# Performance work log

Hardware: AMD Instinct MI355X
Metric: run time of the kernel (lower is better)

The kernel has to match this reference:

```python
import jax, jax.numpy as jnp
import numpy as np

VOCAB = 256
EMB = 512
B, T = 64, 1024


def setup_inputs() -> dict:
    key = jax.random.key(0)
    ks = jax.random.split(key, 7)
    s_emb = 1.0  # nn.Embedding default init N(0,1)
    lim_cell = 1.0 / np.sqrt(2 * EMB)  # Linear default U(-1/sqrt(fan_in), ...)
    lim_head = 1.0 / np.sqrt(EMB)
    return {
        "x": jax.random.randint(ks[0], (B, T), 0, VOCAB),
        "emb": jax.random.normal(ks[1], (VOCAB, EMB), dtype=jnp.float32) * s_emb,
        "w_cell": jax.random.uniform(ks[2], (EMB, 2 * EMB), jnp.float32, -lim_cell, lim_cell),
        "b_cell": jax.random.uniform(ks[3], (EMB,), jnp.float32, -lim_cell, lim_cell),
        "w_head": jax.random.uniform(ks[4], (VOCAB, EMB), jnp.float32, -lim_head, lim_head),
        "b_head": jax.random.uniform(ks[5], (VOCAB,), jnp.float32, -lim_head, lim_head),
        "h0": jnp.zeros((1, EMB), jnp.float32),
    }


def reference(x, emb, w_cell, b_cell, w_head, b_head, h0):
    # x: [B,T] int -> embedded [B,T,E]
    xe = emb[x]
    e = emb.shape[1]
    # cell: tanh(cat(x_t, h) @ W^T + b); split W into x-part and h-part
    w_x, w_h = w_cell[:, :e], w_cell[:, e:]
    # precompute input contribution for all timesteps: [T,B,E]
    xw = jnp.einsum('bte,oe->tbo', xe, w_x) + b_cell
    h_init = jnp.broadcast_to(h0, (xe.shape[0], e))

    def step(h, xw_t):
        h_new = jnp.tanh(xw_t + h @ w_h.T)
        return h_new, h_new

    _, hs = jax.lax.scan(step, h_init, xw)  # hs: [T,B,E]
    hs = jnp.transpose(hs, (1, 0, 2))  # [B,T,E]
    return jnp.einsum('bte,oe->bto', hs, w_head) + b_head
```

## Files before the change

### kernel.cpp

```cpp
#include <hip/hip_runtime.h>

typedef _Float16 h2_t __attribute__((ext_vector_type(2)));
typedef _Float16 h4_t __attribute__((ext_vector_type(4)));
typedef _Float16 h8_t __attribute__((ext_vector_type(8)));
typedef float    f4_t __attribute__((ext_vector_type(4)));
typedef unsigned short u16;

#define EMB   512
#define VOCAB 256
#define NB    64
#define NT    1024

__device__ __forceinline__ float fast_tanh(float z) {
    float e = __expf(2.0f * z);
    return 1.0f - 2.0f / (e + 1.0f);
}

__device__ __forceinline__ unsigned pk2(float a, float b) {
    return __builtin_bit_cast(unsigned, __builtin_amdgcn_cvt_pkrtz(a, b));
}

__global__ __launch_bounds__(256) void prep_kernel(
    const float* __restrict__ emb, const float* __restrict__ w_cell,
    const float* __restrict__ b_cell, const float* __restrict__ w_head,
    u16* __restrict__ embp, unsigned* __restrict__ W2, u16* __restrict__ wh16)
{
    const int blk = blockIdx.x, tid = threadIdx.x;
    if (blk < 256) {
        const int v = blk;
        __shared__ __align__(16) float er[EMB];
        er[tid]       = emb[v * EMB + tid];
        er[tid + 256] = emb[v * EMB + 256 + tid];
        __syncthreads();
        const f4_t* er4 = (const f4_t*)er;
        #pragma unroll
        for (int half = 0; half < 2; ++half) {
            const int o = tid + half * 256;
            const f4_t* wr4 = (const f4_t*)(w_cell + (size_t)o * 1024);
            float s0 = 0.f, s1 = 0.f, s2 = 0.f, s3 = 0.f;
            #pragma unroll 8
            for (int e4 = 0; e4 < 128; ++e4) {
                f4_t w = wr4[e4], a = er4[e4];
                s0 = fmaf(w[0], a[0], s0);
                s1 = fmaf(w[1], a[1], s1);
                s2 = fmaf(w[2], a[2], s2);
                s3 = fmaf(w[3], a[3], s3);
            }
            const float r = (s0 + s1) + (s2 + s3) + b_cell[o];
            embp[v * EMB + o] = __builtin_bit_cast(u16, (_Float16)r);
        }
    } else if (blk < 384) {
        const int base = (blk - 256) * 1024 + tid;
        #pragma unroll
        for (int i = 0; i < 4; ++i) {
            const int P = base + i * 256;
            const int o = P >> 8, p = P & 255;
            h2_t v2;
            v2[0] = (_Float16)w_cell[(size_t)o * 1024 + 512 + 2 * p];
            v2[1] = (_Float16)w_cell[(size_t)o * 1024 + 512 + 2 * p + 1];
            W2[P] = __builtin_bit_cast(unsigned, v2);
        }
    } else {
        const int base = (blk - 384) * 2048 + tid;
        #pragma unroll
        for (int i = 0; i < 8; ++i) {
            const int idx = base + i * 256;
            wh16[idx] = __builtin_bit_cast(u16, (_Float16)w_head[idx]);
        }
    }
}

__global__ __launch_bounds__(512, 2) void rnn_rec(
    const int* __restrict__ x, const float* __restrict__ h0,
    const u16* __restrict__ whf, const u16* __restrict__ embf,
    u16* __restrict__ hs)
{
    extern __shared__ __align__(16) u16 smem[];
    u16* wlds = smem;
    u16* hbuf = smem + 65536;

    const int tid  = threadIdx.x;
    const int wave = tid >> 6, lane = tid & 63;
    const int n    = lane & 15, quad = lane >> 4;
    const int b0   = blockIdx.x * 16;

    #pragma unroll
    for (int g = 0; g < 16; ++g) {
        const int f = g * 512 + tid;
        const int lf = f & 63, If = (f >> 6) & 31, sp = f >> 11;
        const int m = If * 16 + (lf & 15);
        const int k = 384 + sp * 32 + (lf >> 4) * 8;
        *(uint4*)&wlds[(size_t)f * 8] = *(const uint4*)&whf[(size_t)m * 512 + k];
    }

    {
        const u16 u = __builtin_bit_cast(u16, (_Float16)h0[tid]);
        const int e = tid;
        const int ob = ((e >> 5) * 64 + ((e >> 3) & 3) * 16) * 8 + (e & 7);
        #pragma unroll
        for (int nn = 0; nn < 16; ++nn) hbuf[ob + nn * 8] = u;
    }

    h8_t Af[4][12];
    #pragma unroll
    for (int i = 0; i < 4; ++i)
        #pragma unroll
        for (int s = 0; s < 12; ++s)
            Af[i][s] = *(const h8_t*)&whf[(size_t)(((wave << 2) + i) * 16 + n) * EMB
                                          + s * 32 + quad * 8];

    const int* xp  = x  + (size_t)(b0 + n) * NT;
    u16*       hsp = hs + (size_t)(b0 + n) * NT * EMB;

    int eofs[4], wofs[4];
    #pragma unroll
    for (int i = 0; i < 4; ++i) {
        const int I = (wave << 2) + i;
        eofs[i] = I * 16 + (quad << 2);
        const int qq = (2 * I + (quad >> 1)) & 3;
        wofs[i] = ((I >> 1) * 64 + qq * 16 + n) * 8 + (quad & 1) * 4;
    }

    __syncthreads();

    int vB = xp[0];
    h4_t xw_cur[4];
    #pragma unroll
    for (int i = 0; i < 4; ++i)
        xw_cur[i] = *(const h4_t*)&embf[(size_t)vB * EMB + eofs[i]];
    vB = xp[1];

    #pragma unroll 1
    for (int t = 0; t < NT; ++t) {
        const int vC = xp[(t + 2 < NT) ? t + 2 : NT - 1];
        h4_t xw_next[4];
        #pragma unroll
        for (int i = 0; i < 4; ++i)
            xw_next[i] = *(const h4_t*)&embf[(size_t)vB * EMB + eofs[i]];

        const u16* hb = &hbuf[(t & 1) * 8192];
        f4_t acc[4];
        #pragma unroll
        for (int i = 0; i < 4; ++i) {
            acc[i][0] = (float)xw_cur[i][0];
            acc[i][1] = (float)xw_cur[i][1];
            acc[i][2] = (float)xw_cur[i][2];
            acc[i][3] = (float)xw_cur[i][3];
        }

        #pragma unroll
        for (int s = 0; s < 12; ++s) {
            const h8_t bf = *(const h8_t*)&hb[s * 512 + lane * 8];
            #pragma unroll
            for (int i = 0; i < 4; ++i)
                acc[i] = __builtin_amdgcn_mfma_f32_16x16x32_f16(Af[i][s], bf,
                                                                acc[i], 0, 0, 0);
        }
        #pragma unroll
        for (int sp = 0; sp < 4; ++sp) {
            const h8_t bf = *(const h8_t*)&hb[(12 + sp) * 512 + lane * 8];
            #pragma unroll
            for (int i = 0; i < 4; ++i) {
                const int I = (wave << 2) + i;
                const h8_t af = *(const h8_t*)&wlds[((sp * 32 + I) * 64 + lane) * 8];
                acc[i] = __builtin_amdgcn_mfma_f32_16x16x32_f16(af, bf,
                                                                acc[i], 0, 0, 0);
            }
        }

        u16* hw = &hbuf[((t + 1) & 1) * 8192];
        #pragma unroll
        for (int i = 0; i < 4; ++i) {
            const f4_t a = acc[i];
            uint2 pk;
            pk.x = pk2(fast_tanh(a[0]), fast_tanh(a[1]));
            pk.y = pk2(fast_tanh(a[2]), fast_tanh(a[3]));
            *(uint2*)&hw[wofs[i]] = pk;
            *(uint2*)&hsp[(size_t)t * EMB + eofs[i]] = pk;
        }

        vB = vC;
        #pragma unroll
        for (int i = 0; i < 4; ++i) xw_cur[i] = xw_next[i];

        asm volatile("s_waitcnt lgkmcnt(0)\n\ts_barrier" ::: "memory");
    }
}

__global__ __launch_bounds__(512, 2) void head_kernel(
    const u16* __restrict__ hs, const u16* __restrict__ wh16,
    const float* __restrict__ b_head, float* __restrict__ out)
{
    const int tid  = threadIdx.x;
    const int wave = tid >> 6, lane = tid & 63;
    const int l15  = lane & 15, q = lane >> 4;
    const int bt0  = blockIdx.x * 64;

    __shared__ __align__(16) u16 As[64][520];

    {
        const uint4* src = (const uint4*)(hs + (size_t)bt0 * EMB);
        #pragma unroll
        for (int i = 0; i < 8; ++i) {
            const int idx = tid + i * 512;
            const int row = idx >> 6, col8 = idx & 63;
            *(uint4*)&As[row][col8 * 8] = src[idx];
        }
    }

    uint4 bn[16][2];
    #pragma unroll
    for (int i = 0; i < 16; ++i)
        #pragma unroll
        for (int j = 0; j < 2; ++j) {
            const int n = wave * 32 + j * 16 + l15;
            const int k = i * 32 + q * 8;
            bn[i][j] = *(const uint4*)(wh16 + (size_t)n * EMB + k);
        }
    __syncthreads();

    #pragma unroll 1
    for (int mt = 0; mt < 4; ++mt) {
        f4_t acc0 = {0.f, 0.f, 0.f, 0.f}, acc1 = {0.f, 0.f, 0.f, 0.f};
        const int row = mt * 16 + l15;
        #pragma unroll
        for (int i = 0; i < 16; ++i) {
            const int k = i * 32 + q * 8;
            h8_t a = *(const h8_t*)&As[row][k];
            acc0 = __builtin_amdgcn_mfma_f32_16x16x32_f16(
                a, __builtin_bit_cast(h8_t, bn[i][0]), acc0, 0, 0, 0);
            acc1 = __builtin_amdgcn_mfma_f32_16x16x32_f16(
                a, __builtin_bit_cast(h8_t, bn[i][1]), acc1, 0, 0, 0);
        }
        #pragma unroll
        for (int j = 0; j < 2; ++j) {
            const int n = wave * 32 + j * 16 + l15;
            const float bh = b_head[n];
            const f4_t av = j ? acc1 : acc0;
            #pragma unroll
            for (int r = 0; r < 4; ++r) {
                const int orow = bt0 + mt * 16 + q * 4 + r;
                out[(size_t)orow * VOCAB + n] = av[r] + bh;
            }
        }
    }
}

extern "C" void kernel_launch(void* const* d_in, const int* in_sizes, int n_in,
                              void* d_out, int out_size, void* d_ws, size_t ws_size,
                              hipStream_t stream) {
    (void)in_sizes; (void)n_in; (void)out_size; (void)ws_size;
    const int*   x      = (const int*)  d_in[0];
    const float* emb    = (const float*)d_in[1];
    const float* w_cell = (const float*)d_in[2];
    const float* b_cell = (const float*)d_in[3];
    const float* w_head = (const float*)d_in[4];
    const float* b_head = (const float*)d_in[5];
    const float* h0     = (const float*)d_in[6];
    float* out = (float*)d_out;

    char* ws = (char*)d_ws;
    u16*      embf = (u16*)     (ws);
    unsigned* W2   = (unsigned*)(ws + 524288);
    u16*      wh16 = (u16*)     (ws + 1048576);
    u16*      hs   = (u16*)     (ws + 1310720);

    hipFuncSetAttribute((const void*)rnn_rec,
                        hipFuncAttributeMaxDynamicSharedMemorySize, 163840);

    prep_kernel<<<dim3(448), dim3(256), 0, stream>>>(emb, w_cell, b_cell, w_head,
                                                     embf, W2, wh16);
    rnn_rec<<<dim3(4), dim3(512), 163840, stream>>>(x, h0, (const u16*)W2, embf, hs);
    head_kernel<<<dim3((NB * NT) / 64), dim3(512), 0, stream>>>(hs, wh16, b_head, out);
}
```

Before: 3.004 ms.

## Double recurrent block to 1024 threads and keep all recurrent weights in registers

The recurrent kernel now runs 16 waves per block instead of 8, so each wave owns 2 output tiles instead of 4. The full K=512 slice of the recurrent weight fits in registers (2x16 fragments), which removes the LDS-staged weight portion and the large dynamic shared allocation. The aim is to shorten the serial per-timestep critical path by spreading the MFMA work over more waves. In exchange, the per-step barrier now synchronises twice as many waves, and every wave loads all 16 hidden-state fragments from LDS, so total LDS read traffic rises.

```diff
diff --git a/kernel.cpp b/kernel.cpp
--- a/kernel.cpp
+++ b/kernel.cpp
@@ -70,118 +70,103 @@
     }
 }
 
-__global__ __launch_bounds__(512, 2) void rnn_rec(
+__global__ __launch_bounds__(1024, 4) void rnn_rec(
     const int* __restrict__ x, const float* __restrict__ h0,
     const u16* __restrict__ whf, const u16* __restrict__ embf,
     u16* __restrict__ hs)
 {
-    extern __shared__ __align__(16) u16 smem[];
-    u16* wlds = smem;
-    u16* hbuf = smem + 65536;
+    __shared__ __align__(16) u16 hbuf[2][8192];
 
     const int tid  = threadIdx.x;
     const int wave = tid >> 6, lane = tid & 63;
     const int n    = lane & 15, quad = lane >> 4;
     const int b0   = blockIdx.x * 16;
 
-    #pragma unroll
-    for (int g = 0; g < 16; ++g) {
-        const int f = g * 512 + tid;
-        const int lf = f & 63, If = (f >> 6) & 31, sp = f >> 11;
-        const int m = If * 16 + (lf & 15);
-        const int k = 384 + sp * 32 + (lf >> 4) * 8;
-        *(uint4*)&wlds[(size_t)f * 8] = *(const uint4*)&whf[(size_t)m * 512 + k];
-    }
-
-    {
+    if (tid < 512) {
         const u16 u = __builtin_bit_cast(u16, (_Float16)h0[tid]);
         const int e = tid;
         const int ob = ((e >> 5) * 64 + ((e >> 3) & 3) * 16) * 8 + (e & 7);
         #pragma unroll
-        for (int nn = 0; nn < 16; ++nn) hbuf[ob + nn * 8] = u;
-    }
-
-    h8_t Af[4][12];
-    #pragma unroll
-    for (int i = 0; i < 4; ++i)
-        #pragma unroll
-        for (int s = 0; s < 12; ++s)
-            Af[i][s] = *(const h8_t*)&whf[(size_t)(((wave << 2) + i) * 16 + n) * EMB
-                                          + s * 32 + quad * 8];
+        for (int nn = 0; nn < 16; ++nn) hbuf[0][ob + nn * 8] = u;
+    }
+
+    h8_t Af[2][16];
+    #pragma unroll
+    for (int il = 0; il < 2; ++il) {
+        const int I = wave * 2 + il;
+        #pragma unroll
+        for (int s = 0; s < 16; ++s)
+            Af[il][s] = *(const h8_t*)&whf[(size_t)(I * 16 + n) * EMB
+                                           + s * 32 + quad * 8];
+    }
 
     const int* xp  = x  + (size_t)(b0 + n) * NT;
     u16*       hsp = hs + (size_t)(b0 + n) * NT * EMB;
 
-    int eofs[4], wofs[4];
-    #pragma unroll
-    for (int i = 0; i < 4; ++i) {
-        const int I = (wave << 2) + i;
-        eofs[i] = I * 16 + (quad << 2);
+    int eofs[2], wofs[2];
+    #pragma unroll
+    for (int il = 0; il < 2; ++il) {
+        const int I = wave * 2 + il;
+        eofs[il] = I * 16 + (quad << 2);
         const int qq = (2 * I + (quad >> 1)) & 3;
-        wofs[i] = ((I >> 1) * 64 + qq * 16 + n) * 8 + (quad & 1) * 4;
+        wofs[il] = ((I >> 1) * 64 + qq * 16 + n) * 8 + (quad & 1) * 4;
     }
 
     __syncthreads();
 
     int vB = xp[0];
-    h4_t xw_cur[4];
-    #pragma unroll
-    for (int i = 0; i < 4; ++i)
-        xw_cur[i] = *(const h4_t*)&embf[(size_t)vB * EMB + eofs[i]];
+    h4_t xw_cur[2];
+    #pragma unroll
+    for (int il = 0; il < 2; ++il)
+        xw_cur[il] = *(const h4_t*)&embf[(size_t)vB * EMB + eofs[il]];
     vB = xp[1];
 
     #pragma unroll 1
     for (int t = 0; t < NT; ++t) {
         const int vC = xp[(t + 2 < NT) ? t + 2 : NT - 1];
-        h4_t xw_next[4];
-        #pragma unroll
-        for (int i = 0; i < 4; ++i)
-            xw_next[i] = *(const h4_t*)&embf[(size_t)vB * EMB + eofs[i]];
-
-        const u16* hb = &hbuf[(t & 1) * 8192];
-        f4_t acc[4];
-        #pragma unroll
-        for (int i = 0; i < 4; ++i) {
-            acc[i][0] = (float)xw_cur[i][0];
-            acc[i][1] = (float)xw_cur[i][1];
-            acc[i][2] = (float)xw_cur[i][2];
-            acc[i][3] = (float)xw_cur[i][3];
-        }
-
-        #pragma unroll
-        for (int s = 0; s < 12; ++s) {
-            const h8_t bf = *(const h8_t*)&hb[s * 512 + lane * 8];
-            #pragma unroll
-            for (int i = 0; i < 4; ++i)
-                acc[i] = __builtin_amdgcn_mfma_f32_16x16x32_f16(Af[i][s], bf,
-                                                                acc[i], 0, 0, 0);
-        }
-        #pragma unroll
-        for (int sp = 0; sp < 4; ++sp) {
-            const h8_t bf = *(const h8_t*)&hb[(12 + sp) * 512 + lane * 8];
-            #pragma unroll
-            for (int i = 0; i < 4; ++i) {
-                const int I = (wave << 2) + i;
-                const h8_t af = *(const h8_t*)&wlds[((sp * 32 + I) * 64 + lane) * 8];
-                acc[i] = __builtin_amdgcn_mfma_f32_16x16x32_f16(af, bf,
-                                                                acc[i], 0, 0, 0);
-            }
-        }
-
-        u16* hw = &hbuf[((t + 1) & 1) * 8192];
-        #pragma unroll
-        for (int i = 0; i < 4; ++i) {
-            const f4_t a = acc[i];
+        h4_t xw_next[2];
+        #pragma unroll
+        for (int il = 0; il < 2; ++il)
+            xw_next[il] = *(const h4_t*)&embf[(size_t)vB * EMB + eofs[il]];
+
+        const u16* hb = hbuf[t & 1];
+
+        h8_t bf[16];
+        #pragma unroll
+        for (int s = 0; s < 16; ++s)
+            bf[s] = *(const h8_t*)&hb[s * 512 + lane * 8];
+
+        f4_t acc[2];
+        #pragma unroll
+        for (int il = 0; il < 2; ++il) {
+            acc[il][0] = (float)xw_cur[il][0];
+            acc[il][1] = (float)xw_cur[il][1];
+            acc[il][2] = (float)xw_cur[il][2];
+            acc[il][3] = (float)xw_cur[il][3];
+        }
+
+        #pragma unroll
+        for (int s = 0; s < 16; ++s) {
+            acc[0] = __builtin_amdgcn_mfma_f32_16x16x32_f16(Af[0][s], bf[s],
+                                                            acc[0], 0, 0, 0);
+            acc[1] = __builtin_amdgcn_mfma_f32_16x16x32_f16(Af[1][s], bf[s],
+                                                            acc[1], 0, 0, 0);
+        }
+
+        u16* hw = hbuf[(t + 1) & 1];
+        #pragma unroll
+        for (int il = 0; il < 2; ++il) {
+            const f4_t a = acc[il];
             uint2 pk;
             pk.x = pk2(fast_tanh(a[0]), fast_tanh(a[1]));
             pk.y = pk2(fast_tanh(a[2]), fast_tanh(a[3]));
-            *(uint2*)&hw[wofs[i]] = pk;
-            *(uint2*)&hsp[(size_t)t * EMB + eofs[i]] = pk;
+            *(uint2*)&hw[wofs[il]] = pk;
+            *(uint2*)&hsp[(size_t)t * EMB + eofs[il]] = pk;
         }
 
         vB = vC;
         #pragma unroll
-        for (int i = 0; i < 4; ++i) xw_cur[i] = xw_next[i];
+        for (int il = 0; il < 2; ++il) xw_cur[il] = xw_next[il];
 
         asm volatile("s_waitcnt lgkmcnt(0)\n\ts_barrier" ::: "memory");
     }
@@ -265,11 +250,8 @@
     u16*      wh16 = (u16*)     (ws + 1048576);
     u16*      hs   = (u16*)     (ws + 1310720);
 
-    hipFuncSetAttribute((const void*)rnn_rec,
-                        hipFuncAttributeMaxDynamicSharedMemorySize, 163840);
-
     prep_kernel<<<dim3(448), dim3(256), 0, stream>>>(emb, w_cell, b_cell, w_head,
                                                      embf, W2, wh16);
-    rnn_rec<<<dim3(4), dim3(512), 163840, stream>>>(x, h0, (const u16*)W2, embf, hs);
+    rnn_rec<<<dim3(4), dim3(1024), 0, stream>>>(x, h0, (const u16*)W2, embf, hs);
     head_kernel<<<dim3((NB * NT) / 64), dim3(512), 0, stream>>>(hs, wh16, b_head, out);
 }
```

Result: slower. 5.805 ms (+93.2%).
